# Kernel tuning notes

Measured on AMD Instinct MI355X. Metric: run time of the kernel, lower is better.

Reference implementation:

```python
import jax, jax.numpy as jnp
import numpy as np

N, D = 12288, 128
T = 0.07  # temperature from __init__ default


def setup_inputs() -> dict:
    key = jax.random.key(0)
    x = jax.random.normal(key, (N, D), dtype=jnp.float32)
    # L2-normalize rows (this loss is defined on unit-norm embeddings;
    # keeps exp(sim / 0.07) finite in fp32 while preserving the exact math).
    x = x / jnp.linalg.norm(x, axis=-1, keepdims=True)
    return {"x": x}


def reference(x):
    # x: [N, D] -> sim: [N, N]
    sim = jnp.matmul(x, x.T) / T
    # faithful to torch: exp -> sum over last dim -> log -> mean (no LSE stabilization)
    return jnp.mean(jnp.log(jnp.sum(jnp.exp(sim), axis=-1)))
```

## Files before the change

kernel.cpp:

```cpp
#include <hip/hip_runtime.h>
#include <hip/hip_bf16.h>

#define NROWS 12288
#define DDIM  128
#define NT    96
#define CHUNK 6
#define NBLK  816

typedef __bf16 bf16x8 __attribute__((ext_vector_type(8)));
typedef float  f32x4  __attribute__((ext_vector_type(4)));

#define GLD_LDS(g, l) __builtin_amdgcn_global_load_lds(                      \
    (const __attribute__((address_space(1))) void*)(g),                      \
    (__attribute__((address_space(3))) void*)(l), 16, 0, 0)

__device__ __forceinline__ unsigned short f2bf(float f) {
    union { float f; unsigned u; } a; a.f = f;
    unsigned r = a.u + 0x7fffu + ((a.u >> 16) & 1u);
    return (unsigned short)(r >> 16);
}

__global__ void convert_kernel(const float* __restrict__ x, unsigned short* __restrict__ xb,
                               float* __restrict__ rowsum, float* __restrict__ out) {
    int gid = blockIdx.x * 256 + threadIdx.x;
    int i = gid * 4;
    float4 v = *(const float4*)(x + i);
    ushort4 o;
    o.x = f2bf(v.x); o.y = f2bf(v.y); o.z = f2bf(v.z); o.w = f2bf(v.w);
    *(ushort4*)(xb + i) = o;
    if (gid < NROWS) rowsum[gid] = 0.f;
    if (gid == 0) out[0] = 0.f;
}

__global__ __launch_bounds__(256, 4) void gemm_exp_rowsum(
    const unsigned short* __restrict__ xb, float* __restrict__ rowsum)
{
    __shared__ __align__(16) unsigned short smem[128 * DDIM];
    __shared__ float csumS[CHUNK * 128];

    const int tid = threadIdx.x;

    int rem = blockIdx.x, bi = 0;
    for (;;) {
        int nch = (NT - bi + CHUNK - 1) / CHUNK;
        if (rem < nch) break;
        rem -= nch; ++bi;
    }
    const int jt0 = bi + rem * CHUNK;
    const int ntiles = min(CHUNK, NT - jt0);
    const int H = 2 * ntiles;
    const int i0 = bi * 128;

    for (int k = tid; k < CHUNK * 128; k += 256) csumS[k] = 0.f;

    const int wave = tid >> 6, lane = tid & 63;
    const int m16 = lane & 15, q = lane >> 4;

    #pragma unroll
    for (int it = 0; it < 8; ++it) {
        int rbase = wave * 32 + it * 4;
        int r = rbase + (lane >> 4);
        int chunk = (lane & 15) ^ (r & 7);
        GLD_LDS(xb + (size_t)(i0 + r) * DDIM + chunk * 8, smem + rbase * DDIM);
    }
    __syncthreads();

    bf16x8 af[2][4];
    #pragma unroll
    for (int mi = 0; mi < 2; ++mi) {
        int r = wave * 32 + mi * 16 + m16;
        #pragma unroll
        for (int ks = 0; ks < 4; ++ks)
            af[mi][ks] = *(const bf16x8*)(&smem[r * DDIM + (((ks * 4 + q) ^ (r & 7)) * 8)]);
    }
    __syncthreads();

    unsigned short* const buf0 = smem;
    unsigned short* const buf1 = smem + 64 * DDIM;

    #define STAGE_HALF(h, dst) do {                                              \
        int jrow0_ = jt0 * 128 + (h) * 64;                                       \
        _Pragma("unroll")                                                        \
        for (int it = 0; it < 4; ++it) {                                         \
            int rbase = wave * 16 + it * 4;                                      \
            int r = rbase + (lane >> 4);                                         \
            int chunk = (lane & 15) ^ (r & 7);                                   \
            GLD_LDS(xb + (size_t)(jrow0_ + r) * DDIM + chunk * 8, (dst) + rbase * DDIM); \
        }                                                                        \
    } while (0)

    STAGE_HALF(0, buf0);

    const float SCALE = 20.609929155556625f;

    f32x4 rp4[2];
    rp4[0] = (f32x4){0.f, 0.f, 0.f, 0.f};
    rp4[1] = (f32x4){0.f, 0.f, 0.f, 0.f};

    for (int h = 0; h < H; ++h) {
        __syncthreads();
        unsigned short* nxt = ((h + 1) & 1) ? buf1 : buf0;
        if (h + 1 < H) STAGE_HALF(h + 1, nxt);

        const unsigned short* cb = (h & 1) ? buf1 : buf0;

        f32x4 acc[2][4] = {};
        #pragma unroll
        for (int ks = 0; ks < 4; ++ks) {
            bf16x8 bfr[4];
            #pragma unroll
            for (int ni = 0; ni < 4; ++ni) {
                int r = ni * 16 + m16;
                bfr[ni] = *(const bf16x8*)(&cb[r * DDIM + (((ks * 4 + q) ^ (r & 7)) * 8)]);
            }
            __builtin_amdgcn_s_setprio(1);
            #pragma unroll
            for (int mi = 0; mi < 2; ++mi)
                #pragma unroll
                for (int ni = 0; ni < 4; ++ni)
                    acc[mi][ni] = __builtin_amdgcn_mfma_f32_16x16x32_bf16(
                        af[mi][ks], bfr[ni], acc[mi][ni], 0, 0, 0);
            __builtin_amdgcn_s_setprio(0);
        }

        float cp[4] = {0.f, 0.f, 0.f, 0.f};
        #pragma unroll
        for (int mi = 0; mi < 2; ++mi)
            #pragma unroll
            for (int ni = 0; ni < 4; ++ni) {
                f32x4 sv = acc[mi][ni] * SCALE;
                f32x4 ev;
                ev[0] = __builtin_amdgcn_exp2f(sv[0]);
                ev[1] = __builtin_amdgcn_exp2f(sv[1]);
                ev[2] = __builtin_amdgcn_exp2f(sv[2]);
                ev[3] = __builtin_amdgcn_exp2f(sv[3]);
                rp4[mi] += ev;
                cp[ni] += (ev[0] + ev[1]) + (ev[2] + ev[3]);
            }

        if (jt0 + (h >> 1) != bi) {
            #pragma unroll
            for (int ni = 0; ni < 4; ++ni) {
                float s = cp[ni];
                s += __shfl_xor(s, 16);
                s += __shfl_xor(s, 32);
                if (q == 0) atomicAdd(&csumS[h * 64 + ni * 16 + m16], s);
            }
        }
    }

    #pragma unroll
    for (int mi = 0; mi < 2; ++mi)
        #pragma unroll
        for (int r = 0; r < 4; ++r) {
            float s = rp4[mi][r];
            s += __shfl_xor(s, 1);
            s += __shfl_xor(s, 2);
            s += __shfl_xor(s, 4);
            s += __shfl_xor(s, 8);
            if (m16 == 0) atomicAdd(&rowsum[i0 + wave * 32 + mi * 16 + q * 4 + r], s);
        }

    __syncthreads();
    for (int k = tid; k < ntiles * 128; k += 256) {
        float v = csumS[k];
        if (v != 0.f) atomicAdd(&rowsum[jt0 * 128 + k], v);
    }
}

__global__ void finalize_kernel(const float* __restrict__ rowsum, float* __restrict__ out) {
    __shared__ float red[4];
    int gid = blockIdx.x * 256 + threadIdx.x;
    float lg = __logf(rowsum[gid]);
    #pragma unroll
    for (int off = 1; off < 64; off <<= 1)
        lg += __shfl_xor(lg, off);
    const int wv = threadIdx.x >> 6, ln = threadIdx.x & 63;
    if (ln == 0) red[wv] = lg;
    __syncthreads();
    if (threadIdx.x == 0)
        atomicAdd(out, (red[0] + red[1] + red[2] + red[3]) * (1.0f / (float)NROWS));
}

extern "C" void kernel_launch(void* const* d_in, const int* in_sizes, int n_in,
                              void* d_out, int out_size, void* d_ws, size_t ws_size,
                              hipStream_t stream) {
    const float* x = (const float*)d_in[0];
    float* out = (float*)d_out;

    float* rowsum = (float*)d_ws;
    unsigned short* xb = (unsigned short*)((char*)d_ws + NROWS * sizeof(float));

    convert_kernel<<<dim3((NROWS * DDIM) / (4 * 256)), dim3(256), 0, stream>>>(x, xb, rowsum, out);
    gemm_exp_rowsum<<<dim3(NBLK), dim3(256), 0, stream>>>(xb, rowsum);
    finalize_kernel<<<dim3(NROWS / 256), dim3(256), 0, stream>>>(rowsum, out);
}
```

Before: 104.4 us.

## Prefetch two stages ahead with explicit vmcnt waits instead of full syncthreads

```diff
diff --git a/kernel.cpp b/kernel.cpp
--- a/kernel.cpp
+++ b/kernel.cpp
@@ -63,7 +63,8 @@
         int chunk = (lane & 15) ^ (r & 7);
         GLD_LDS(xb + (size_t)(i0 + r) * DDIM + chunk * 8, smem + rbase * DDIM);
     }
-    __syncthreads();
+    asm volatile("s_waitcnt vmcnt(0)" ::: "memory");
+    __builtin_amdgcn_s_barrier();
 
     bf16x8 af[2][4];
     #pragma unroll
@@ -73,23 +74,24 @@
         for (int ks = 0; ks < 4; ++ks)
             af[mi][ks] = *(const bf16x8*)(&smem[r * DDIM + (((ks * 4 + q) ^ (r & 7)) * 8)]);
     }
-    __syncthreads();
-
-    unsigned short* const buf0 = smem;
-    unsigned short* const buf1 = smem + 64 * DDIM;
-
-    #define STAGE_HALF(h, dst) do {                                              \
+    asm volatile("s_waitcnt lgkmcnt(0)" ::: "memory");
+    __builtin_amdgcn_sched_barrier(0);
+    __builtin_amdgcn_s_barrier();
+
+    #define STAGE_HALF(h) do {                                                   \
+        unsigned short* dst_ = smem + ((h) & 1) * (64 * DDIM);                   \
         int jrow0_ = jt0 * 128 + (h) * 64;                                       \
         _Pragma("unroll")                                                        \
         for (int it = 0; it < 4; ++it) {                                         \
             int rbase = wave * 16 + it * 4;                                      \
             int r = rbase + (lane >> 4);                                         \
             int chunk = (lane & 15) ^ (r & 7);                                   \
-            GLD_LDS(xb + (size_t)(jrow0_ + r) * DDIM + chunk * 8, (dst) + rbase * DDIM); \
+            GLD_LDS(xb + (size_t)(jrow0_ + r) * DDIM + chunk * 8, dst_ + rbase * DDIM); \
         }                                                                        \
     } while (0)
 
-    STAGE_HALF(0, buf0);
+    STAGE_HALF(0);
+    STAGE_HALF(1);
 
     const float SCALE = 20.609929155556625f;
 
@@ -98,11 +100,11 @@
     rp4[1] = (f32x4){0.f, 0.f, 0.f, 0.f};
 
     for (int h = 0; h < H; ++h) {
-        __syncthreads();
-        unsigned short* nxt = ((h + 1) & 1) ? buf1 : buf0;
-        if (h + 1 < H) STAGE_HALF(h + 1, nxt);
-
-        const unsigned short* cb = (h & 1) ? buf1 : buf0;
+        if (h + 1 < H) asm volatile("s_waitcnt vmcnt(4)" ::: "memory");
+        else           asm volatile("s_waitcnt vmcnt(0)" ::: "memory");
+        __builtin_amdgcn_s_barrier();
+
+        const unsigned short* cb = smem + (h & 1) * (64 * DDIM);
 
         f32x4 acc[2][4] = {};
         #pragma unroll
@@ -123,7 +125,10 @@
             __builtin_amdgcn_s_setprio(0);
         }
 
-        float cp[4] = {0.f, 0.f, 0.f, 0.f};
+        f32x4 cp4[4];
+        #pragma unroll
+        for (int ni = 0; ni < 4; ++ni) cp4[ni] = (f32x4){0.f, 0.f, 0.f, 0.f};
+
         #pragma unroll
         for (int mi = 0; mi < 2; ++mi)
             #pragma unroll
@@ -135,18 +140,22 @@
                 ev[2] = __builtin_amdgcn_exp2f(sv[2]);
                 ev[3] = __builtin_amdgcn_exp2f(sv[3]);
                 rp4[mi] += ev;
-                cp[ni] += (ev[0] + ev[1]) + (ev[2] + ev[3]);
+                cp4[ni] += ev;
             }
 
         if (jt0 + (h >> 1) != bi) {
             #pragma unroll
             for (int ni = 0; ni < 4; ++ni) {
-                float s = cp[ni];
+                float s = (cp4[ni][0] + cp4[ni][1]) + (cp4[ni][2] + cp4[ni][3]);
                 s += __shfl_xor(s, 16);
                 s += __shfl_xor(s, 32);
                 if (q == 0) atomicAdd(&csumS[h * 64 + ni * 16 + m16], s);
             }
         }
+
+        __builtin_amdgcn_s_barrier();
+        __builtin_amdgcn_sched_barrier(0);
+        if (h + 2 < H) STAGE_HALF(h + 2);
     }
 
     #pragma unroll
@@ -166,6 +175,7 @@
         float v = csumS[k];
         if (v != 0.f) atomicAdd(&rowsum[jt0 * 128 + k], v);
     }
+    #undef STAGE_HALF
 }
 
 __global__ void finalize_kernel(const float* __restrict__ rowsum, float* __restrict__ out) {
```

Measured after the change: 104.1 us. Within noise of the previous version (-0.2%).
